# Optimization experiments

Hardware: AMD Instinct MI355X
Metric: run time of the kernel (lower is better)

Reference implementation:

```python
import jax, jax.numpy as jnp
import numpy as np
from jax import lax

N = 2048        # nodes
F_IN = 512      # input features
D_MODEL = 256
D_INNER = 256   # must equal d_model (shapes in original forward)
DT_RANK = 16
N_STATE = 16    # block ssm state size
LAYER_NUM = 8   # GCN propagation depth == ssm seq len
NUM_CLASSES = 40
HDIM = 8; NHEADS = D_MODEL // HDIM; D_ST2 = 8; D_CONV = 4   # Mamba2 branch
CONV_DIM = D_INNER + 2 * D_ST2
ALPHA = 0.1; GW = 0.5
BN_EPS = 1e-5; RMS_EPS = 1e-5

def setup_inputs():
    key = jax.random.key(0)
    ks = jax.random.split(key, 16)
    def uni(k, shape, s):
        return jax.random.uniform(k, shape, minval=-s, maxval=s, dtype=jnp.float32)
    d_in_proj = 2 * D_INNER + 2 * D_ST2 + NHEADS
    blk_A = jnp.tile(jnp.arange(1, N_STATE + 1, dtype=jnp.float32)[None, :], (D_INNER, 1))
    return {
        "x": jax.random.normal(ks[0], (N, F_IN), dtype=jnp.float32),
        "adj": jax.random.normal(ks[1], (N, N), dtype=jnp.float32) * (0.5 / np.sqrt(N)),
        "lin1_W": uni(ks[2], (F_IN, D_MODEL), 1.0 / np.sqrt(D_MODEL)),
        "m2_in_proj": uni(ks[3], (D_MODEL, d_in_proj), 1.0 / np.sqrt(D_MODEL)),
        "m2_conv_w": uni(ks[4], (CONV_DIM, D_CONV), 1.0 / np.sqrt(D_CONV)),
        "m2_conv_b": jnp.zeros((CONV_DIM,), jnp.float32),
        "m2_dt_bias": uni(ks[5], (NHEADS,), 0.1),
        "m2_A_log": jnp.log(jnp.arange(1, NHEADS + 1, dtype=jnp.float32)),
        "m2_D": jnp.ones((NHEADS,), jnp.float32),
        "m2_norm_w": jnp.ones((D_INNER,), jnp.float32),
        "m2_out_proj": uni(ks[6], (D_INNER, D_MODEL), 1.0 / np.sqrt(D_MODEL)),
        "blk_xproj_W": uni(ks[7], (D_INNER, DT_RANK + 2 * N_STATE), 1.0 / np.sqrt(DT_RANK + 2 * N_STATE)),
        "blk_dtproj_W": uni(ks[8], (DT_RANK, D_INNER), 1.0 / np.sqrt(D_INNER)),
        "blk_A_log": jnp.log(blk_A),
        "blk_D": jnp.ones((D_INNER,), jnp.float32),
        "blk_outproj_W": uni(ks[9], (D_INNER, D_MODEL), 1.0 / np.sqrt(D_MODEL)),
        "bn1_g": jnp.ones((D_MODEL,), jnp.float32),
        "bn1_b": jnp.zeros((D_MODEL,), jnp.float32),
        "bn2_g": jnp.ones((D_MODEL,), jnp.float32),
        "bn2_b": jnp.zeros((D_MODEL,), jnp.float32),
        "lin2_W": uni(ks[10], (D_MODEL, NUM_CLASSES), 1.0 / np.sqrt(NUM_CLASSES)),
    }

def _bn_eval(x, g, b):
    # eval-mode BatchNorm1d with fresh running stats (mean=0, var=1)
    return x * (g / np.sqrt(1.0 + BN_EPS)) + b

def _mamba2(u, in_proj, conv_w, conv_b, dt_bias, A_log, Dp, norm_w, out_proj):
    # u: (b, l, d_model). Mamba2 with expand=1, ngroups=1, headdim=8, d_state=8.
    b, l, _ = u.shape
    zxbcdt = u @ in_proj
    z = zxbcdt[..., :D_INNER]
    xBC = zxbcdt[..., D_INNER:D_INNER + CONV_DIM]
    dt = jax.nn.softplus(zxbcdt[..., -NHEADS:] + dt_bias)          # (b,l,h)
    # causal depthwise conv over sequence
    conv = lax.conv_general_dilated(
        xBC.transpose(0, 2, 1), conv_w[:, None, :], (1,), [(D_CONV - 1, 0)],
        feature_group_count=CONV_DIM)
    xBC = jax.nn.silu(conv.transpose(0, 2, 1) + conv_b)
    xh = xBC[..., :D_INNER].reshape(b, l, NHEADS, HDIM)
    Bm = xBC[..., D_INNER:D_INNER + D_ST2]                          # (b,l,n)
    Cm = xBC[..., D_INNER + D_ST2:]                                 # (b,l,n)
    A = -jnp.exp(A_log)                                             # (h,)
    dA = jnp.exp(dt * A)                                            # (b,l,h)
    dBx = jnp.einsum('blh,bln,blhp->blhpn', dt, Bm, xh)
    def step(s, inp):
        dA_t, dBx_t, C_t = inp
        s = dA_t[:, :, None, None] * s + dBx_t                      # (b,h,p,n)
        return s, jnp.einsum('bhpn,bn->bhp', s, C_t)
    s0 = jnp.zeros((b, NHEADS, HDIM, D_ST2), u.dtype)
    _, ys = lax.scan(step, s0, (dA.transpose(1, 0, 2),
                                dBx.transpose(1, 0, 2, 3, 4),
                                Cm.transpose(1, 0, 2)))
    y = ys.transpose(1, 0, 2, 3) + xh * Dp[None, None, :, None]
    y = y.reshape(b, l, D_INNER)
    g = y * jax.nn.silu(z)                                          # gated RMSNorm
    g = g * lax.rsqrt(jnp.mean(g * g, -1, keepdims=True) + RMS_EPS) * norm_w
    return g @ out_proj

def _gcn_mamba_block(xb, adj, xproj_W, dtproj_W, A_log, Dp, outproj_W):
    # GCN propagation builds the 'sequence' over layers; Mamba selective scan over it.
    feats = [xb]
    xi = xb
    for _ in range(LAYER_NUM - 1):
        xi = adj @ xi
        xi = 0.95 * xi + 0.05 * xb     # alpha=0.05 hardcoded in original forward
        feats.append(xi)
    xs = jnp.stack(feats, axis=1)                                   # (N, L, d)
    x_dbl = jax.nn.relu(xs @ xproj_W)
    delta = jax.nn.softplus(x_dbl[..., :DT_RANK] @ dtproj_W)        # (N,L,d)
    Bm = x_dbl[..., DT_RANK:DT_RANK + N_STATE]
    Cm = x_dbl[..., DT_RANK + N_STATE:]
    A = -jnp.exp(A_log)                                             # (d,n)
    dA = jnp.exp(jnp.einsum('bld,dn->bldn', delta, A))
    dBu = jnp.einsum('bld,bln,bld->bldn', delta, Bm, xs)
    def step(s, inp):
        dA_t, dBu_t, C_t = inp
        s = dA_t * s + dBu_t                                        # (N,d,n)
        return s, jnp.einsum('bdn,bn->bd', s, C_t)
    s0 = jnp.zeros((xs.shape[0], D_INNER, N_STATE), xs.dtype)
    _, ys = lax.scan(step, s0, (dA.transpose(1, 0, 2, 3),
                                dBu.transpose(1, 0, 2, 3),
                                Cm.transpose(1, 0, 2)))
    y = ys.transpose(1, 0, 2) + xs * Dp
    return y @ outproj_W                                            # (N,L,d_model)

def reference(x, adj, lin1_W, m2_in_proj, m2_conv_w, m2_conv_b, m2_dt_bias,
              m2_A_log, m2_D, m2_norm_w, m2_out_proj, blk_xproj_W, blk_dtproj_W,
              blk_A_log, blk_D, blk_outproj_W, bn1_g, bn1_b, bn2_g, bn2_b, lin2_W):
    x_input = x @ lin1_W                                            # (N,d)
    g_in = x_input[None]                                            # (1,N,d)
    m2 = lambda t: _mamba2(t, m2_in_proj, m2_conv_w, m2_conv_b, m2_dt_bias,
                           m2_A_log, m2_D, m2_norm_w, m2_out_proj)
    g_out = m2(g_in) + jnp.flip(m2(jnp.flip(g_in, 1)), 1)
    g_out = jax.nn.relu(g_out)[0] * (1.0 - ALPHA) + ALPHA * x_input
    xb = jax.nn.relu(_bn_eval(x_input, bn1_g, bn1_b))
    all_out = _gcn_mamba_block(xb, adj, blk_xproj_W, blk_dtproj_W,
                               blk_A_log, blk_D, blk_outproj_W)
    output = (all_out[:, -1, :] + x_input) * GW + g_out * (1.0 - GW)
    output = jax.nn.relu(_bn_eval(output, bn2_g, bn2_b))
    all_out = jax.nn.relu(all_out)
    y = output @ lin2_W
    return (all_out, jax.nn.log_softmax(y, axis=-1))
```

## Files before the change

kernel.cpp:

```cpp
#include <hip/hip_runtime.h>
#include <math.h>


typedef _Float16 half8 __attribute__((ext_vector_type(8)));
typedef _Float16 half4v __attribute__((ext_vector_type(4)));
typedef float f32x4 __attribute__((ext_vector_type(4)));

__device__ __forceinline__ float softplus_fast(float x) {
    return fmaxf(x, 0.f) + __logf(1.f + __expf(-fabsf(x)));
}
__device__ __forceinline__ float silu_fast(float x) {
    return __fdividef(x, 1.f + __expf(-x));
}

template<int EPI>
__global__ __launch_bounds__(256) void mm16(
    const _Float16* __restrict__ A16, int lda,
    const _Float16* __restrict__ BT16, int ldb,
    float* __restrict__ dst, _Float16* __restrict__ dst16,
    const float* __restrict__ aux, float* __restrict__ aux2,
    int N, int ldc, int kchunk)
{
    __shared__ _Float16 As[128][40];
    __shared__ _Float16 Bs[64][40];
    const int tid = threadIdx.x;
    const int col0 = blockIdx.x * 64;
    const int row0 = blockIdx.y * 128;
    const int kz = blockIdx.z;
    const int k0 = kz * kchunk;
    const int wave = tid >> 6, lane = tid & 63;
    f32x4 acc[2][4];
    #pragma unroll
    for (int i = 0; i < 2; ++i)
        #pragma unroll
        for (int j = 0; j < 4; ++j)
            acc[i][j] = (f32x4){0.f, 0.f, 0.f, 0.f};
    const int ar = tid >> 1, ac = (tid & 1) * 16;
    const int br = tid >> 2, bc = (tid & 3) * 8;
    const int lrow = lane & 15, kof = (lane >> 4) * 8;
    for (int ks = 0; ks < kchunk; ks += 32) {
        {
            const _Float16* src = A16 + (size_t)(row0 + ar) * lda + k0 + ks + ac;
            *reinterpret_cast<float4*>(&As[ar][ac])     = *reinterpret_cast<const float4*>(src);
            *reinterpret_cast<float4*>(&As[ar][ac + 8]) = *reinterpret_cast<const float4*>(src + 8);
        }
        {
            const _Float16* src = BT16 + (size_t)(col0 + br) * ldb + k0 + ks + bc;
            *reinterpret_cast<float4*>(&Bs[br][bc]) = *reinterpret_cast<const float4*>(src);
        }
        __syncthreads();
        half8 a[2], b[4];
        #pragma unroll
        for (int fr = 0; fr < 2; ++fr)
            a[fr] = *reinterpret_cast<const half8*>(&As[wave * 32 + fr * 16 + lrow][kof]);
        #pragma unroll
        for (int fc = 0; fc < 4; ++fc)
            b[fc] = *reinterpret_cast<const half8*>(&Bs[fc * 16 + lrow][kof]);
        #pragma unroll
        for (int fr = 0; fr < 2; ++fr)
            #pragma unroll
            for (int fc = 0; fc < 4; ++fc)
                acc[fr][fc] = __builtin_amdgcn_mfma_f32_16x16x32_f16(a[fr], b[fc], acc[fr][fc], 0, 0, 0);
        __syncthreads();
    }
    const int col = lane & 15, rbase = (lane >> 4) * 4;
    #pragma unroll
    for (int fr = 0; fr < 2; ++fr)
        #pragma unroll
        for (int fc = 0; fc < 4; ++fc) {
            int c = col0 + fc * 16 + col;
            #pragma unroll
            for (int i = 0; i < 4; ++i) {
                int m = row0 + wave * 32 + fr * 16 + rbase + i;
                float v = acc[fr][fc][i];
                if (EPI == 0) {
                    float* P = dst + (size_t)kz * gridDim.y * 128 * 256;
                    P[(size_t)m * 256 + c] = v;
                } else if (EPI == 1) {
                    if (c < N) dst[(size_t)m * ldc + c] = fmaxf(v, 0.f);
                } else if (EPI == 2) {
                    dst[(size_t)m * 256 + c] = fmaxf(v, 0.f) * 0.9f + 0.1f * aux[(size_t)m * 256 + c];
                } else if (EPI == 3) {
                    int bb = m & 2047, ll = m >> 11;
                    dst[(size_t)((bb << 3) + ll) * 256 + c] = fmaxf(v, 0.f);
                    if (ll == 7) aux2[(size_t)bb * 256 + c] = v;
                } else if (EPI == 4) {
                    dst[(size_t)m * 256 + c] = v;
                    dst16[(size_t)m * 256 + c] = (_Float16)v;
                } else {
                    if (c < N) dst[(size_t)m * ldc + c] = v;
                }
            }
        }
}

__global__ __launch_bounds__(256) void k_cvt16(
    const float* __restrict__ in, _Float16* __restrict__ o)
{
    int i = (blockIdx.x * 256 + threadIdx.x) * 4;
    float4 v = *reinterpret_cast<const float4*>(&in[i]);
    half4v h;
    h[0] = (_Float16)v.x; h[1] = (_Float16)v.y; h[2] = (_Float16)v.z; h[3] = (_Float16)v.w;
    *reinterpret_cast<half4v*>(&o[i]) = h;
}

__global__ __launch_bounds__(256) void k_wt16(
    const float* __restrict__ w, _Float16* __restrict__ o, int K, int N)
{
    int idx = blockIdx.x * 256 + threadIdx.x;
    int n = idx / K, k = idx - n * K;
    o[idx] = (n < N) ? (_Float16)w[(size_t)k * N + n] : (_Float16)0.f;
}

__global__ __launch_bounds__(256) void k_xb_t16(
    const float* __restrict__ X, const float* __restrict__ g, const float* __restrict__ b,
    float* __restrict__ xb, _Float16* __restrict__ f16a, _Float16* __restrict__ fT16)
{
    const float sc = 0.99999500003749951f;
    int m0 = (blockIdx.x >> 3) * 32, n0 = (blockIdx.x & 7) * 32;
    int tx = threadIdx.x & 31, tg = threadIdx.x >> 5;
    __shared__ float T[32][33];
    float gd = g[n0 + tx] * sc, bd = b[n0 + tx];
    #pragma unroll
    for (int i = 0; i < 4; ++i) {
        int m = tg * 4 + i;
        size_t idx = (size_t)(m0 + m) * 256 + n0 + tx;
        float v = fmaxf(X[idx] * gd + bd, 0.f);
        xb[idx] = v;
        f16a[idx] = (_Float16)v;
        T[m][tx] = v;
    }
    __syncthreads();
    #pragma unroll
    for (int j = 0; j < 4; ++j) {
        int n = tg * 4 + j;
        fT16[(size_t)(n0 + n) * 2048 + m0 + tx] = (_Float16)T[tx][n];
    }
}

__global__ __launch_bounds__(256) void k_combine_t16(
    const float* __restrict__ psum, const float* __restrict__ xb,
    float* __restrict__ xi, _Float16* __restrict__ xi16, _Float16* __restrict__ fT16)
{
    int m0 = (blockIdx.x >> 3) * 32, n0 = (blockIdx.x & 7) * 32;
    int tx = threadIdx.x & 31, tg = threadIdx.x >> 5;
    __shared__ float T[32][33];
    #pragma unroll
    for (int i = 0; i < 4; ++i) {
        int m = tg * 4 + i;
        size_t idx = (size_t)(m0 + m) * 256 + n0 + tx;
        float s = psum[idx];
        #pragma unroll
        for (int q = 1; q < 8; ++q) s += psum[idx + (size_t)q * 524288];
        float v = 0.95f * s + 0.05f * xb[idx];
        xi[idx] = v;
        xi16[idx] = (_Float16)v;
        T[m][tx] = v;
    }
    __syncthreads();
    #pragma unroll
    for (int j = 0; j < 4; ++j) {
        int n = tg * 4 + j;
        fT16[(size_t)(n0 + n) * 2048 + m0 + tx] = (_Float16)T[tx][n];
    }
}

__global__ __launch_bounds__(256) void k_dtda(
    const float* __restrict__ Z, const float* __restrict__ bias,
    const float* __restrict__ A_log, float* __restrict__ dt, float* __restrict__ dA)
{
    int idx = blockIdx.x * 256 + threadIdx.x;
    if (idx >= 2048 * 32) return;
    int t = idx >> 5, h = idx & 31;
    float v = Z[(size_t)t * 560 + 528 + h] + bias[h];
    float dtv = softplus_fast(v);
    float Ah = -__expf(A_log[h]);
    dt[idx] = dtv;
    dA[idx] = __expf(dtv * Ah);
}

__global__ __launch_bounds__(320) void k_conv(
    const float* __restrict__ Z, const float* __restrict__ w, const float* __restrict__ bconv,
    float* __restrict__ xhf, float* __restrict__ Bf, float* __restrict__ Cf,
    float* __restrict__ xhr, float* __restrict__ Br, float* __restrict__ Cr)
{
    int bx = blockIdx.x;
    int dir = bx >> 11, t = bx & 2047;
    int c = threadIdx.x;
    if (c >= 272) return;
    float acc = bconv[c];
    #pragma unroll
    for (int k = 0; k < 4; ++k) {
        int tt = dir ? (t + 3 - k) : (t - 3 + k);
        if (tt >= 0 && tt < 2048) acc = fmaf(w[c * 4 + k], Z[(size_t)tt * 560 + 256 + c], acc);
    }
    float v = silu_fast(acc);
    float* xh = dir ? xhr : xhf;
    float* B  = dir ? Br  : Bf;
    float* C  = dir ? Cr  : Cf;
    if (c < 256)       xh[(size_t)t * 256 + c] = v;
    else if (c < 264)  B[(size_t)t * 8 + (c - 256)] = v;
    else               C[(size_t)t * 8 + (c - 264)] = v;
}

__global__ __launch_bounds__(64) void k_scan_m2_p1(
    const float* __restrict__ dt, const float* __restrict__ dA,
    const float* __restrict__ xhf, const float* __restrict__ Bf, const float* __restrict__ Cf,
    const float* __restrict__ xhr, const float* __restrict__ Br, const float* __restrict__ Cr,
    const float* __restrict__ Dvec,
    float* __restrict__ yf, float* __restrict__ yr,
    float* __restrict__ Ptbuf,
    float* __restrict__ Acbuf,
    float* __restrict__ Sloc)
{
    int bid = blockIdx.x;
    int c  = bid & 31;
    int hh = bid >> 5;
    int dir = hh >> 5, h = hh & 31;
    const float* xhp = dir ? xhr : xhf;
    const float* Bp  = dir ? Br  : Bf;
    const float* Cp  = dir ? Cr  : Cf;
    float* yp        = dir ? yr  : yf;
    int lane = threadIdx.x;
    int p = lane >> 3, n = lane & 7;
    float Dh = Dvec[h];
    __shared__ float dAs[64];
    __shared__ float Ps[64][8];
    __shared__ float Bs[64][8];
    __shared__ float Cs[64][8];
    __shared__ float Ys[64][8];
    __shared__ float Pts[64];
    const int j0 = c * 64;
    {
        int j = j0 + lane;
        int t = dir ? (2047 - j) : j;
        dAs[lane] = dA[(size_t)t * 32 + h];
    }
    #pragma unroll
    for (int q = 0; q < 8; ++q) {
        int idx = q * 64 + lane;
        int i = idx >> 3, e = idx & 7;
        int j = j0 + i;
        int t = dir ? (2047 - j) : j;
        Ps[i][e] = dt[(size_t)t * 32 + h] * xhp[(size_t)t * 256 + h * 8 + e];
        Bs[i][e] = Bp[(size_t)t * 8 + e];
        Cs[i][e] = Cp[(size_t)t * 8 + e];
    }
    __syncthreads();
    float s = 0.f;
    float P = 1.f;
    for (int i = 0; i < 64; ++i) {
        float a = dAs[i];
        float u = Ps[i][p] * Bs[i][n];
        s = fmaf(a, s, u);
        P *= a;
        float yv = s * Cs[i][n];
        yv += __shfl_xor(yv, 1);
        yv += __shfl_xor(yv, 2);
        yv += __shfl_xor(yv, 4);
        if (n == 0) Ys[i][p] = yv;
        if (lane == 0) Pts[i] = P;
    }
    __syncthreads();
    #pragma unroll
    for (int q = 0; q < 8; ++q) {
        int idx = q * 64 + lane;
        int i = idx >> 3, e = idx & 7;
        int j = j0 + i;
        int t = dir ? (2047 - j) : j;
        yp[(size_t)t * 256 + h * 8 + e] = Ys[i][e] + xhp[(size_t)t * 256 + h * 8 + e] * Dh;
    }
    {
        int j = j0 + lane;
        Ptbuf[((size_t)dir * 2048 + j) * 32 + h] = Pts[lane];
    }
    if (lane == 0) Acbuf[hh * 32 + c] = P;
    Sloc[((size_t)hh * 32 + c) * 64 + lane] = s;
}

__global__ __launch_bounds__(64) void k_scan_m2_p2(
    const float* __restrict__ Acbuf, const float* __restrict__ Sloc,
    float* __restrict__ Sstart)
{
    int hh = blockIdx.x;
    int lane = threadIdx.x;
    float s = 0.f;
    for (int c = 0; c < 32; ++c) {
        Sstart[((size_t)hh * 32 + c) * 64 + lane] = s;
        float a = Acbuf[hh * 32 + c];
        s = fmaf(a, s, Sloc[((size_t)hh * 32 + c) * 64 + lane]);
    }
}

__global__ __launch_bounds__(256) void k_gate(
    const float* __restrict__ Z, const float* __restrict__ yf, const float* __restrict__ yr,
    const float* __restrict__ Cf, const float* __restrict__ Cr,
    const float* __restrict__ Ptbuf, const float* __restrict__ Sstart,
    const float* __restrict__ nw, float* __restrict__ gsum, _Float16* __restrict__ gsum16)
{
    int t = blockIdx.x, d = threadIdx.x;
    int h = d >> 3, p = d & 7;
    __shared__ float Csh[2][8];
    if (d < 8)       Csh[0][d] = Cf[(size_t)t * 8 + d];
    else if (d < 16) Csh[1][d - 8] = Cr[(size_t)t * 8 + (d - 8)];
    __syncthreads();
    int jf = t, jr = 2047 - t;
    int cf = jf >> 6, cr = jr >> 6;
    float Ptf = Ptbuf[((size_t)jf) * 32 + h];
    float Ptr = Ptbuf[((size_t)2048 + jr) * 32 + h];
    const float* ssf = &Sstart[(((size_t)h) * 32 + cf) * 64 + p * 8];
    const float* ssr = &Sstart[(((size_t)(32 + h)) * 32 + cr) * 64 + p * 8];
    float dotf = 0.f, dotr = 0.f;
    #pragma unroll
    for (int n2 = 0; n2 < 8; ++n2) {
        dotf = fmaf(ssf[n2], Csh[0][n2], dotf);
        dotr = fmaf(ssr[n2], Csh[1][n2], dotr);
    }
    float yfv = yf[(size_t)t * 256 + d] + Ptf * dotf;
    float yrv = yr[(size_t)t * 256 + d] + Ptr * dotr;
    float zv = Z[(size_t)t * 560 + d];
    float sz = silu_fast(zv);
    float gf = yfv * sz;
    float gr = yrv * sz;
    float vf = gf * gf, vr = gr * gr;
    for (int o = 32; o > 0; o >>= 1) { vf += __shfl_down(vf, o); vr += __shfl_down(vr, o); }
    __shared__ float sfa[4], sra[4];
    __shared__ float tot[2];
    int wid = d >> 6;
    if ((d & 63) == 0) { sfa[wid] = vf; sra[wid] = vr; }
    __syncthreads();
    if (d == 0) {
        tot[0] = sfa[0] + sfa[1] + sfa[2] + sfa[3];
        tot[1] = sra[0] + sra[1] + sra[2] + sra[3];
    }
    __syncthreads();
    float inf_ = rsqrtf(tot[0] / 256.f + 1e-5f);
    float inr_ = rsqrtf(tot[1] / 256.f + 1e-5f);
    float g = (gf * inf_ + gr * inr_) * nw[d];
    gsum[(size_t)t * 256 + d] = g;
    gsum16[(size_t)t * 256 + d] = (_Float16)g;
}

__global__ __launch_bounds__(256) void k_scan_gcn(
    const float* __restrict__ xdbl,
    const float* __restrict__ dtW,
    const float* __restrict__ A_log,
    const float* __restrict__ Dv,
    float* __restrict__ feats,
    _Float16* __restrict__ f16o)
{
    int b = blockIdx.x, d = threadIdx.x;
    __shared__ float xrow[8][48];
    for (int j = d; j < 384; j += 256) {
        int l = j / 48, k = j % 48;
        xrow[l][k] = xdbl[(size_t)(l * 2048 + b) * 48 + k];
    }
    __syncthreads();
    float a[16];
    #pragma unroll
    for (int n = 0; n < 16; ++n) a[n] = -__expf(A_log[d * 16 + n]);
    float Dd = Dv[d];
    float s[16];
    #pragma unroll
    for (int n = 0; n < 16; ++n) s[n] = 0.f;
    for (int l = 0; l < 8; ++l) {
        float accd = 0.f;
        #pragma unroll
        for (int k = 0; k < 16; ++k) accd = fmaf(xrow[l][k], dtW[k * 256 + d], accd);
        float dl = softplus_fast(accd);
        size_t r = (size_t)(l * 2048 + b) * 256 + d;
        float xv = feats[r];
        float du = dl * xv;
        float y = 0.f;
        #pragma unroll
        for (int n = 0; n < 16; ++n) {
            float dAn = __expf(dl * a[n]);
            s[n] = fmaf(dAn, s[n], du * xrow[l][16 + n]);
            y = fmaf(s[n], xrow[l][32 + n], y);
        }
        float res = y + xv * Dd;
        feats[r] = res;
        f16o[r] = (_Float16)res;
    }
}

__global__ __launch_bounds__(256) void k_head(
    const float* __restrict__ lastl, const float* __restrict__ X, const float* __restrict__ gout,
    const float* __restrict__ g2, const float* __restrict__ b2, const float* __restrict__ W2,
    float* __restrict__ out1)
{
    int b = blockIdx.x, d = threadIdx.x;
    __shared__ float ov[256];
    __shared__ float yv[40];
    const float sc = 0.99999500003749951f;
    float v = (lastl[(size_t)b * 256 + d] + X[(size_t)b * 256 + d]) * 0.5f
              + gout[(size_t)b * 256 + d] * 0.5f;
    v = v * (g2[d] * sc) + b2[d];
    ov[d] = fmaxf(v, 0.f);
    __syncthreads();
    if (d < 40) {
        float acc = 0.f;
        for (int k = 0; k < 256; ++k) acc = fmaf(ov[k], W2[k * 40 + d], acc);
        yv[d] = acc;
    }
    __syncthreads();
    if (d < 40) {
        float m = -1e30f;
        for (int j = 0; j < 40; ++j) m = fmaxf(m, yv[j]);
        float se = 0.f;
        for (int j = 0; j < 40; ++j) se += expf(yv[j] - m);
        out1[(size_t)b * 40 + d] = yv[d] - m - logf(se);
    }
}

extern "C" void kernel_launch(void* const* d_in, const int* in_sizes, int n_in,
                              void* d_out, int out_size, void* d_ws, size_t ws_size,
                              hipStream_t stream)
{
    const float* x      = (const float*)d_in[0];
    const float* adj    = (const float*)d_in[1];
    const float* lin1W  = (const float*)d_in[2];
    const float* inproj = (const float*)d_in[3];
    const float* convw  = (const float*)d_in[4];
    const float* convb  = (const float*)d_in[5];
    const float* dtbias = (const float*)d_in[6];
    const float* m2Alog = (const float*)d_in[7];
    const float* m2D    = (const float*)d_in[8];
    const float* normw  = (const float*)d_in[9];
    const float* outprj = (const float*)d_in[10];
    const float* xprojW = (const float*)d_in[11];
    const float* dtprjW = (const float*)d_in[12];
    const float* bAlog  = (const float*)d_in[13];
    const float* bD     = (const float*)d_in[14];
    const float* boutW  = (const float*)d_in[15];
    const float* bn1g   = (const float*)d_in[16];
    const float* bn1b   = (const float*)d_in[17];
    const float* bn2g   = (const float*)d_in[18];
    const float* bn2b   = (const float*)d_in[19];
    const float* lin2W  = (const float*)d_in[20];
    float* out = (float*)d_out;
    float* ws  = (float*)d_ws;

    float* X     = ws + 0;
    float* Z     = ws + 524288;
    float* dt    = ws + 1671168;
    float* dA    = ws + 1736704;
    float* xhf   = ws + 1802240;
    float* Bf    = ws + 2326528;
    float* Cf    = ws + 2342912;
    float* xhr   = ws + 2359296;
    float* Br    = ws + 2883584;
    float* Cr    = ws + 2899968;
    float* yf    = ws + 2916352;
    float* yr    = ws + 3440640;
    float* gsum  = ws + 3964928;
    float* gout  = ws + 4489216;
    float* feats = ws + 5013504;
    float* xdbl  = ws + 9207808;
    float* lastl = ws + 9994240;
    float* psum  = ws + 10518528;
    _Float16* adj16h    = (_Float16*)(ws + 14712832);
    _Float16* fT16h     = (_Float16*)(ws + 16809984);
    _Float16* WT16h     = (_Float16*)(ws + 17072128);
    _Float16* x16       = (_Float16*)(ws + 17104896);
    _Float16* lin1WT16  = (_Float16*)(ws + 17629184);
    _Float16* inprojT16 = (_Float16*)(ws + 17694720);
    _Float16* outprjT16 = (_Float16*)(ws + 17768448);
    _Float16* xprojT16  = (_Float16*)(ws + 17801216);
    _Float16* X16       = (_Float16*)(ws + 17809408);
    _Float16* gsum16    = (_Float16*)(ws + 18071552);
    _Float16* feats16a  = (_Float16*)(ws + 18333696);
    float* Ptbuf  = psum;
    float* Acbuf  = psum + 131072;
    float* Sloc   = psum + 133120;
    float* Sstart = psum + 264192;
    (void)ws_size; (void)in_sizes; (void)n_in; (void)out_size;

    dim3 blk(256);
    k_cvt16<<<dim3(1024), blk, 0, stream>>>(x, x16);
    k_cvt16<<<dim3(4096), blk, 0, stream>>>(adj, adj16h);
    k_wt16<<<dim3(512),  blk, 0, stream>>>(lin1W,  lin1WT16, 512, 256);
    k_wt16<<<dim3(576),  blk, 0, stream>>>(inproj, inprojT16, 256, 560);
    k_wt16<<<dim3(256),  blk, 0, stream>>>(outprj, outprjT16, 256, 256);
    k_wt16<<<dim3(64),   blk, 0, stream>>>(xprojW, xprojT16, 256, 48);
    k_wt16<<<dim3(256),  blk, 0, stream>>>(boutW,  WT16h, 256, 256);
    mm16<4><<<dim3(4, 16, 1), blk, 0, stream>>>(x16, 512, lin1WT16, 512, X, X16, nullptr, nullptr, 256, 256, 512);
    mm16<5><<<dim3(9, 16, 1), blk, 0, stream>>>(X16, 256, inprojT16, 256, Z, nullptr, nullptr, nullptr, 560, 560, 256);
    k_dtda<<<dim3(256), blk, 0, stream>>>(Z, dtbias, m2Alog, dt, dA);
    k_conv<<<dim3(4096), dim3(320), 0, stream>>>(Z, convw, convb, xhf, Bf, Cf, xhr, Br, Cr);
    k_scan_m2_p1<<<dim3(2048), dim3(64), 0, stream>>>(dt, dA, xhf, Bf, Cf, xhr, Br, Cr, m2D,
                                                      yf, yr, Ptbuf, Acbuf, Sloc);
    k_scan_m2_p2<<<dim3(64), dim3(64), 0, stream>>>(Acbuf, Sloc, Sstart);
    k_gate<<<dim3(2048), blk, 0, stream>>>(Z, yf, yr, Cf, Cr, Ptbuf, Sstart, normw, gsum, gsum16);
    mm16<2><<<dim3(4, 16, 1), blk, 0, stream>>>(gsum16, 256, outprjT16, 256, gout, nullptr, X, nullptr, 256, 256, 256);
    k_xb_t16<<<dim3(512), blk, 0, stream>>>(X, bn1g, bn1b, feats, feats16a, fT16h);
    for (int i = 1; i < 8; ++i) {
        mm16<0><<<dim3(4, 16, 8), blk, 0, stream>>>(adj16h, 2048, fT16h, 2048, psum, nullptr, nullptr, nullptr, 256, 256, 256);
        k_combine_t16<<<dim3(512), blk, 0, stream>>>(psum, feats, feats + (size_t)i * 524288,
                                                     feats16a + (size_t)i * 524288, fT16h);
    }
    mm16<1><<<dim3(1, 128, 1), blk, 0, stream>>>(feats16a, 256, xprojT16, 256, xdbl, nullptr, nullptr, nullptr, 48, 48, 256);
    k_scan_gcn<<<dim3(2048), blk, 0, stream>>>(xdbl, dtprjW, bAlog, bD, feats, feats16a);
    mm16<3><<<dim3(4, 128, 1), blk, 0, stream>>>(feats16a, 256, WT16h, 256, out, nullptr, nullptr, lastl, 256, 256, 256);
    k_head<<<dim3(2048), blk, 0, stream>>>(lastl, X, gout, bn2g, bn2b, lin2W, out + 4194304);
}
```

Baseline: 259.6 us.

## Fuse GCN propagation split-K matmul with combine and merge prep kernels

Result: slower. 305.8 us (+17.8%).

```diff
diff --git a/kernel.cpp b/kernel.cpp
--- a/kernel.cpp
+++ b/kernel.cpp
@@ -26,8 +26,6 @@
     const int tid = threadIdx.x;
     const int col0 = blockIdx.x * 64;
     const int row0 = blockIdx.y * 128;
-    const int kz = blockIdx.z;
-    const int k0 = kz * kchunk;
     const int wave = tid >> 6, lane = tid & 63;
     f32x4 acc[2][4];
     #pragma unroll
@@ -40,12 +38,12 @@
     const int lrow = lane & 15, kof = (lane >> 4) * 8;
     for (int ks = 0; ks < kchunk; ks += 32) {
         {
-            const _Float16* src = A16 + (size_t)(row0 + ar) * lda + k0 + ks + ac;
+            const _Float16* src = A16 + (size_t)(row0 + ar) * lda + ks + ac;
             *reinterpret_cast<float4*>(&As[ar][ac])     = *reinterpret_cast<const float4*>(src);
             *reinterpret_cast<float4*>(&As[ar][ac + 8]) = *reinterpret_cast<const float4*>(src + 8);
         }
         {
-            const _Float16* src = BT16 + (size_t)(col0 + br) * ldb + k0 + ks + bc;
+            const _Float16* src = BT16 + (size_t)(col0 + br) * ldb + ks + bc;
             *reinterpret_cast<float4*>(&Bs[br][bc]) = *reinterpret_cast<const float4*>(src);
         }
         __syncthreads();
@@ -73,10 +71,7 @@
             for (int i = 0; i < 4; ++i) {
                 int m = row0 + wave * 32 + fr * 16 + rbase + i;
                 float v = acc[fr][fc][i];
-                if (EPI == 0) {
-                    float* P = dst + (size_t)kz * gridDim.y * 128 * 256;
-                    P[(size_t)m * 256 + c] = v;
-                } else if (EPI == 1) {
+                if (EPI == 1) {
                     if (c < N) dst[(size_t)m * ldc + c] = fmaxf(v, 0.f);
                 } else if (EPI == 2) {
                     dst[(size_t)m * 256 + c] = fmaxf(v, 0.f) * 0.9f + 0.1f * aux[(size_t)m * 256 + c];
@@ -94,27 +89,106 @@
         }
 }
 
-__global__ __launch_bounds__(256) void k_cvt16(
-    const float* __restrict__ in, _Float16* __restrict__ o)
-{
-    int i = (blockIdx.x * 256 + threadIdx.x) * 4;
-    float4 v = *reinterpret_cast<const float4*>(&in[i]);
-    half4v h;
-    h[0] = (_Float16)v.x; h[1] = (_Float16)v.y; h[2] = (_Float16)v.z; h[3] = (_Float16)v.w;
-    *reinterpret_cast<half4v*>(&o[i]) = h;
-}
-
-__global__ __launch_bounds__(256) void k_wt16(
-    const float* __restrict__ w, _Float16* __restrict__ o, int K, int N)
-{
-    int idx = blockIdx.x * 256 + threadIdx.x;
-    int n = idx / K, k = idx - n * K;
-    o[idx] = (n < N) ? (_Float16)w[(size_t)k * N + n] : (_Float16)0.f;
+__global__ __launch_bounds__(256) void k_chain(
+    const _Float16* __restrict__ adj16,
+    const _Float16* __restrict__ ftin,
+    const _Float16* __restrict__ xb16,
+    _Float16* __restrict__ xi16,
+    _Float16* __restrict__ ftout)
+{
+    __shared__ _Float16 As[64][40];
+    __shared__ _Float16 Bs[64][40];
+    const int tid = threadIdx.x;
+    const int col0 = blockIdx.x * 64;
+    const int row0 = blockIdx.y * 64;
+    const int wave = tid >> 6, lane = tid & 63;
+    f32x4 acc[4];
+    #pragma unroll
+    for (int j = 0; j < 4; ++j) acc[j] = (f32x4){0.f, 0.f, 0.f, 0.f};
+    const int ar = tid >> 2, ac = (tid & 3) * 8;
+    const int lrow = lane & 15, kof = (lane >> 4) * 8;
+    float4 pa = *reinterpret_cast<const float4*>(adj16 + (size_t)(row0 + ar) * 2048 + ac);
+    float4 pb = *reinterpret_cast<const float4*>(ftin  + (size_t)(col0 + ar) * 2048 + ac);
+    for (int ks = 0; ks < 2048; ks += 32) {
+        *reinterpret_cast<float4*>(&As[ar][ac]) = pa;
+        *reinterpret_cast<float4*>(&Bs[ar][ac]) = pb;
+        __syncthreads();
+        if (ks + 32 < 2048) {
+            pa = *reinterpret_cast<const float4*>(adj16 + (size_t)(row0 + ar) * 2048 + ks + 32 + ac);
+            pb = *reinterpret_cast<const float4*>(ftin  + (size_t)(col0 + ar) * 2048 + ks + 32 + ac);
+        }
+        half8 a = *reinterpret_cast<const half8*>(&As[wave * 16 + lrow][kof]);
+        half8 b[4];
+        #pragma unroll
+        for (int fc = 0; fc < 4; ++fc)
+            b[fc] = *reinterpret_cast<const half8*>(&Bs[fc * 16 + lrow][kof]);
+        #pragma unroll
+        for (int fc = 0; fc < 4; ++fc)
+            acc[fc] = __builtin_amdgcn_mfma_f32_16x16x32_f16(a, b[fc], acc[fc], 0, 0, 0);
+        __syncthreads();
+    }
+    const int col = lane & 15, rbase = (lane >> 4) * 4;
+    const int mbase = row0 + wave * 16 + rbase;
+    #pragma unroll
+    for (int fc = 0; fc < 4; ++fc) {
+        int c = col0 + fc * 16 + col;
+        half4v hv;
+        #pragma unroll
+        for (int i = 0; i < 4; ++i) {
+            float v = 0.95f * acc[fc][i] + 0.05f * (float)xb16[(size_t)(mbase + i) * 256 + c];
+            xi16[(size_t)(mbase + i) * 256 + c] = (_Float16)v;
+            hv[i] = (_Float16)v;
+        }
+        *reinterpret_cast<half4v*>(ftout + (size_t)c * 2048 + mbase) = hv;
+    }
+}
+
+__global__ __launch_bounds__(256) void k_prep(
+    const float* __restrict__ x, const float* __restrict__ adj,
+    const float* __restrict__ lin1W, const float* __restrict__ inproj,
+    const float* __restrict__ outprj, const float* __restrict__ xprojW,
+    const float* __restrict__ boutW,
+    _Float16* __restrict__ x16, _Float16* __restrict__ adj16,
+    _Float16* __restrict__ lin1WT, _Float16* __restrict__ inprojT,
+    _Float16* __restrict__ outprjT, _Float16* __restrict__ xprojT,
+    _Float16* __restrict__ WT16)
+{
+    int b = blockIdx.x, tid = threadIdx.x;
+    if (b < 5120) {
+        const float* src = (b < 1024) ? x : adj;
+        _Float16* o = (b < 1024) ? x16 : adj16;
+        int lb = (b < 1024) ? b : b - 1024;
+        int i = (lb * 256 + tid) * 4;
+        float4 v = *reinterpret_cast<const float4*>(&src[i]);
+        half4v h;
+        h[0] = (_Float16)v.x; h[1] = (_Float16)v.y; h[2] = (_Float16)v.z; h[3] = (_Float16)v.w;
+        *reinterpret_cast<half4v*>(&o[i]) = h;
+    } else if (b < 5632) {
+        int idx = (b - 5120) * 256 + tid;
+        int n = idx >> 9, k = idx & 511;
+        lin1WT[idx] = (_Float16)lin1W[(size_t)k * 256 + n];
+    } else if (b < 6208) {
+        int idx = (b - 5632) * 256 + tid;
+        int n = idx >> 8, k = idx & 255;
+        inprojT[idx] = (n < 560) ? (_Float16)inproj[(size_t)k * 560 + n] : (_Float16)0.f;
+    } else if (b < 6464) {
+        int idx = (b - 6208) * 256 + tid;
+        int n = idx >> 8, k = idx & 255;
+        outprjT[idx] = (_Float16)outprj[(size_t)k * 256 + n];
+    } else if (b < 6528) {
+        int idx = (b - 6464) * 256 + tid;
+        int n = idx >> 8, k = idx & 255;
+        xprojT[idx] = (n < 48) ? (_Float16)xprojW[(size_t)k * 48 + n] : (_Float16)0.f;
+    } else {
+        int idx = (b - 6528) * 256 + tid;
+        int n = idx >> 8, k = idx & 255;
+        WT16[idx] = (_Float16)boutW[(size_t)k * 256 + n];
+    }
 }
 
 __global__ __launch_bounds__(256) void k_xb_t16(
     const float* __restrict__ X, const float* __restrict__ g, const float* __restrict__ b,
-    float* __restrict__ xb, _Float16* __restrict__ f16a, _Float16* __restrict__ fT16)
+    _Float16* __restrict__ f16a, _Float16* __restrict__ fT16)
 {
     const float sc = 0.99999500003749951f;
     int m0 = (blockIdx.x >> 3) * 32, n0 = (blockIdx.x & 7) * 32;
@@ -126,7 +200,6 @@
         int m = tg * 4 + i;
         size_t idx = (size_t)(m0 + m) * 256 + n0 + tx;
         float v = fmaxf(X[idx] * gd + bd, 0.f);
-        xb[idx] = v;
         f16a[idx] = (_Float16)v;
         T[m][tx] = v;
     }
@@ -136,47 +209,6 @@
         int n = tg * 4 + j;
         fT16[(size_t)(n0 + n) * 2048 + m0 + tx] = (_Float16)T[tx][n];
     }
-}
-
-__global__ __launch_bounds__(256) void k_combine_t16(
-    const float* __restrict__ psum, const float* __restrict__ xb,
-    float* __restrict__ xi, _Float16* __restrict__ xi16, _Float16* __restrict__ fT16)
-{
-    int m0 = (blockIdx.x >> 3) * 32, n0 = (blockIdx.x & 7) * 32;
-    int tx = threadIdx.x & 31, tg = threadIdx.x >> 5;
-    __shared__ float T[32][33];
-    #pragma unroll
-    for (int i = 0; i < 4; ++i) {
-        int m = tg * 4 + i;
-        size_t idx = (size_t)(m0 + m) * 256 + n0 + tx;
-        float s = psum[idx];
-        #pragma unroll
-        for (int q = 1; q < 8; ++q) s += psum[idx + (size_t)q * 524288];
-        float v = 0.95f * s + 0.05f * xb[idx];
-        xi[idx] = v;
-        xi16[idx] = (_Float16)v;
-        T[m][tx] = v;
-    }
-    __syncthreads();
-    #pragma unroll
-    for (int j = 0; j < 4; ++j) {
-        int n = tg * 4 + j;
-        fT16[(size_t)(n0 + n) * 2048 + m0 + tx] = (_Float16)T[tx][n];
-    }
-}
-
-__global__ __launch_bounds__(256) void k_dtda(
-    const float* __restrict__ Z, const float* __restrict__ bias,
-    const float* __restrict__ A_log, float* __restrict__ dt, float* __restrict__ dA)
-{
-    int idx = blockIdx.x * 256 + threadIdx.x;
-    if (idx >= 2048 * 32) return;
-    int t = idx >> 5, h = idx & 31;
-    float v = Z[(size_t)t * 560 + 528 + h] + bias[h];
-    float dtv = softplus_fast(v);
-    float Ah = -__expf(A_log[h]);
-    dt[idx] = dtv;
-    dA[idx] = __expf(dtv * Ah);
 }
 
 __global__ __launch_bounds__(320) void k_conv(
@@ -204,7 +236,7 @@
 }
 
 __global__ __launch_bounds__(64) void k_scan_m2_p1(
-    const float* __restrict__ dt, const float* __restrict__ dA,
+    const float* __restrict__ Z, const float* __restrict__ dtbias, const float* __restrict__ A_log,
     const float* __restrict__ xhf, const float* __restrict__ Bf, const float* __restrict__ Cf,
     const float* __restrict__ xhr, const float* __restrict__ Br, const float* __restrict__ Cr,
     const float* __restrict__ Dvec,
@@ -224,6 +256,7 @@
     int lane = threadIdx.x;
     int p = lane >> 3, n = lane & 7;
     float Dh = Dvec[h];
+    __shared__ float dts[64];
     __shared__ float dAs[64];
     __shared__ float Ps[64][8];
     __shared__ float Bs[64][8];
@@ -234,15 +267,19 @@
     {
         int j = j0 + lane;
         int t = dir ? (2047 - j) : j;
-        dAs[lane] = dA[(size_t)t * 32 + h];
-    }
+        float v = Z[(size_t)t * 560 + 528 + h] + dtbias[h];
+        float dtv = softplus_fast(v);
+        dts[lane] = dtv;
+        dAs[lane] = __expf(-dtv * __expf(A_log[h]));
+    }
+    __syncthreads();
     #pragma unroll
     for (int q = 0; q < 8; ++q) {
         int idx = q * 64 + lane;
         int i = idx >> 3, e = idx & 7;
         int j = j0 + i;
         int t = dir ? (2047 - j) : j;
-        Ps[i][e] = dt[(size_t)t * 32 + h] * xhp[(size_t)t * 256 + h * 8 + e];
+        Ps[i][e] = dts[i] * xhp[(size_t)t * 256 + h * 8 + e];
         Bs[i][e] = Bp[(size_t)t * 8 + e];
         Cs[i][e] = Cp[(size_t)t * 8 + e];
     }
@@ -346,8 +383,7 @@
     const float* __restrict__ dtW,
     const float* __restrict__ A_log,
     const float* __restrict__ Dv,
-    float* __restrict__ feats,
-    _Float16* __restrict__ f16o)
+    _Float16* __restrict__ f16io)
 {
     int b = blockIdx.x, d = threadIdx.x;
     __shared__ float xrow[8][48];
@@ -369,7 +405,7 @@
         for (int k = 0; k < 16; ++k) accd = fmaf(xrow[l][k], dtW[k * 256 + d], accd);
         float dl = softplus_fast(accd);
         size_t r = (size_t)(l * 2048 + b) * 256 + d;
-        float xv = feats[r];
+        float xv = (float)f16io[r];
         float du = dl * xv;
         float y = 0.f;
         #pragma unroll
@@ -378,9 +414,7 @@
             s[n] = fmaf(dAn, s[n], du * xrow[l][16 + n]);
             y = fmaf(s[n], xrow[l][32 + n], y);
         }
-        float res = y + xv * Dd;
-        feats[r] = res;
-        f16o[r] = (_Float16)res;
+        f16io[r] = (_Float16)(y + xv * Dd);
     }
 }
 
@@ -443,8 +477,6 @@
 
     float* X     = ws + 0;
     float* Z     = ws + 524288;
-    float* dt    = ws + 1671168;
-    float* dA    = ws + 1736704;
     float* xhf   = ws + 1802240;
     float* Bf    = ws + 2326528;
     float* Cf    = ws + 2342912;
@@ -455,12 +487,16 @@
     float* yr    = ws + 3440640;
     float* gsum  = ws + 3964928;
     float* gout  = ws + 4489216;
-    float* feats = ws + 5013504;
     float* xdbl  = ws + 9207808;
     float* lastl = ws + 9994240;
-    float* psum  = ws + 10518528;
+    float* scr   = ws + 10518528;
+    float* Ptbuf  = scr;
+    float* Acbuf  = scr + 131072;
+    float* Sloc   = scr + 133120;
+    float* Sstart = scr + 264192;
+    _Float16* fT16B     = (_Float16*)(ws + 5013504);
     _Float16* adj16h    = (_Float16*)(ws + 14712832);
-    _Float16* fT16h     = (_Float16*)(ws + 16809984);
+    _Float16* fT16A     = (_Float16*)(ws + 16809984);
     _Float16* WT16h     = (_Float16*)(ws + 17072128);
     _Float16* x16       = (_Float16*)(ws + 17104896);
     _Float16* lin1WT16  = (_Float16*)(ws + 17629184);
@@ -470,37 +506,32 @@
     _Float16* X16       = (_Float16*)(ws + 17809408);
     _Float16* gsum16    = (_Float16*)(ws + 18071552);
     _Float16* feats16a  = (_Float16*)(ws + 18333696);
-    float* Ptbuf  = psum;
-    float* Acbuf  = psum + 131072;
-    float* Sloc   = psum + 133120;
-    float* Sstart = psum + 264192;
     (void)ws_size; (void)in_sizes; (void)n_in; (void)out_size;
 
     dim3 blk(256);
-    k_cvt16<<<dim3(1024), blk, 0, stream>>>(x, x16);
-    k_cvt16<<<dim3(4096), blk, 0, stream>>>(adj, adj16h);
-    k_wt16<<<dim3(512),  blk, 0, stream>>>(lin1W,  lin1WT16, 512, 256);
-    k_wt16<<<dim3(576),  blk, 0, stream>>>(inproj, inprojT16, 256, 560);
-    k_wt16<<<dim3(256),  blk, 0, stream>>>(outprj, outprjT16, 256, 256);
-    k_wt16<<<dim3(64),   blk, 0, stream>>>(xprojW, xprojT16, 256, 48);
-    k_wt16<<<dim3(256),  blk, 0, stream>>>(boutW,  WT16h, 256, 256);
-    mm16<4><<<dim3(4, 16, 1), blk, 0, stream>>>(x16, 512, lin1WT16, 512, X, X16, nullptr, nullptr, 256, 256, 512);
-    mm16<5><<<dim3(9, 16, 1), blk, 0, stream>>>(X16, 256, inprojT16, 256, Z, nullptr, nullptr, nullptr, 560, 560, 256);
-    k_dtda<<<dim3(256), blk, 0, stream>>>(Z, dtbias, m2Alog, dt, dA);
+    k_prep<<<dim3(6784), blk, 0, stream>>>(x, adj, lin1W, inproj, outprj, xprojW, boutW,
+                                           x16, adj16h, lin1WT16, inprojT16, outprjT16,
+                                           xprojT16, WT16h);
+    mm16<4><<<dim3(4, 16), blk, 0, stream>>>(x16, 512, lin1WT16, 512, X, X16, nullptr, nullptr, 256, 256, 512);
+    mm16<5><<<dim3(9, 16), blk, 0, stream>>>(X16, 256, inprojT16, 256, Z, nullptr, nullptr, nullptr, 560, 560, 256);
     k_conv<<<dim3(4096), dim3(320), 0, stream>>>(Z, convw, convb, xhf, Bf, Cf, xhr, Br, Cr);
-    k_scan_m2_p1<<<dim3(2048), dim3(64), 0, stream>>>(dt, dA, xhf, Bf, Cf, xhr, Br, Cr, m2D,
-                                                      yf, yr, Ptbuf, Acbuf, Sloc);
+    k_scan_m2_p1<<<dim3(2048), dim3(64), 0, stream>>>(Z, dtbias, m2Alog, xhf, Bf, Cf, xhr, Br, Cr,
+                                                      m2D, yf, yr, Ptbuf, Acbuf, Sloc);
     k_scan_m2_p2<<<dim3(64), dim3(64), 0, stream>>>(Acbuf, Sloc, Sstart);
     k_gate<<<dim3(2048), blk, 0, stream>>>(Z, yf, yr, Cf, Cr, Ptbuf, Sstart, normw, gsum, gsum16);
-    mm16<2><<<dim3(4, 16, 1), blk, 0, stream>>>(gsum16, 256, outprjT16, 256, gout, nullptr, X, nullptr, 256, 256, 256);
-    k_xb_t16<<<dim3(512), blk, 0, stream>>>(X, bn1g, bn1b, feats, feats16a, fT16h);
-    for (int i = 1; i < 8; ++i) {
-        mm16<0><<<dim3(4, 16, 8), blk, 0, stream>>>(adj16h, 2048, fT16h, 2048, psum, nullptr, nullptr, nullptr, 256, 256, 256);
-        k_combine_t16<<<dim3(512), blk, 0, stream>>>(psum, feats, feats + (size_t)i * 524288,
-                                                     feats16a + (size_t)i * 524288, fT16h);
-    }
-    mm16<1><<<dim3(1, 128, 1), blk, 0, stream>>>(feats16a, 256, xprojT16, 256, xdbl, nullptr, nullptr, nullptr, 48, 48, 256);
-    k_scan_gcn<<<dim3(2048), blk, 0, stream>>>(xdbl, dtprjW, bAlog, bD, feats, feats16a);
-    mm16<3><<<dim3(4, 128, 1), blk, 0, stream>>>(feats16a, 256, WT16h, 256, out, nullptr, nullptr, lastl, 256, 256, 256);
+    mm16<2><<<dim3(4, 16), blk, 0, stream>>>(gsum16, 256, outprjT16, 256, gout, nullptr, X, nullptr, 256, 256, 256);
+    k_xb_t16<<<dim3(512), blk, 0, stream>>>(X, bn1g, bn1b, feats16a, fT16A);
+    {
+        _Float16* p = fT16A;
+        _Float16* q = fT16B;
+        for (int i = 1; i < 8; ++i) {
+            k_chain<<<dim3(4, 32), blk, 0, stream>>>(adj16h, p, feats16a,
+                                                     feats16a + (size_t)i * 524288, q);
+            _Float16* tmp = p; p = q; q = tmp;
+        }
+    }
+    mm16<1><<<dim3(1, 128), blk, 0, stream>>>(feats16a, 256, xprojT16, 256, xdbl, nullptr, nullptr, nullptr, 48, 48, 256);
+    k_scan_gcn<<<dim3(2048), blk, 0, stream>>>(xdbl, dtprjW, bAlog, bD, feats16a);
+    mm16<3><<<dim3(4, 128), blk, 0, stream>>>(feats16a, 256, WT16h, 256, out, nullptr, nullptr, lastl, 256, 256, 256);
     k_head<<<dim3(2048), blk, 0, stream>>>(lastl, X, gout, bn2g, bn2b, lin2W, out + 4194304);
 }
```
